# Kernel optimization log

Hardware: AMD Instinct MI355X
Metric: run time of the kernel (lower is better)

## Reference

```python
import jax, jax.numpy as jnp
import numpy as np

N_SYS = 512      # number of crystal systems in the batch
N_ATOM = 32      # atoms per system (uniform for the reference)
N = N_SYS * N_ATOM            # 16384 total atoms
M = N_SYS * N_ATOM * N_ATOM   # 524288 dense intra-system edges
R = 16           # lattice translation points per edge
E = 128          # embed_dim
H = 8            # num_heads


def setup_inputs() -> dict:
    key = jax.random.key(0)
    ks = jax.random.split(key, 6)
    x = jax.random.normal(ks[0], (N, E), jnp.float32)
    in_proj_weight = jax.random.normal(ks[1], (3 * E, E), jnp.float32) / np.float32(np.sqrt(E))
    in_proj_bias = jnp.zeros((3 * E,), jnp.float32)
    out_proj_weight = jax.random.normal(ks[2], (E, E), jnp.float32) / np.float32(np.sqrt(E))
    out_proj_bias = jnp.zeros((E,), jnp.float32)
    # per-node per-head Gaussian exponents; must be negative for convergent lattice sums
    alpha = -(jax.random.uniform(ks[3], (N, H), jnp.float32) * 0.9 + 0.1)
    # squared distances from atom i to lattice images of atom j, up to ~5 Angstrom
    dist2 = jax.random.uniform(ks[4], (M, R), jnp.float32) * 25.0
    # dense intra-system edge list in (query-major) block order, as Crystalformer assumes
    base = (np.arange(N_SYS, dtype=np.int32) * N_ATOM)[:, None, None]
    qi = np.arange(N_ATOM, dtype=np.int32)[None, :, None]
    kj = np.arange(N_ATOM, dtype=np.int32)[None, None, :]
    e0 = np.broadcast_to(base + qi, (N_SYS, N_ATOM, N_ATOM)).reshape(-1)
    e1 = np.broadcast_to(base + kj, (N_SYS, N_ATOM, N_ATOM)).reshape(-1)
    edges = jnp.asarray(np.stack([e0, e1]), jnp.int32)
    batch = jnp.asarray(np.repeat(np.arange(N_SYS, dtype=np.int32), N_ATOM))
    return {
        "x": x,
        "in_proj_weight": in_proj_weight,
        "in_proj_bias": in_proj_bias,
        "out_proj_weight": out_proj_weight,
        "out_proj_bias": out_proj_bias,
        "alpha": alpha,
        "dist2": dist2,
        "edges": edges,
        "batch": batch,
    }


def reference(x, in_proj_weight, in_proj_bias, out_proj_weight, out_proj_bias,
              alpha, dist2, edges, batch):
    n, e = x.shape
    h = alpha.shape[1]
    dh = e // h
    # in-projection (self-attention: q = k = v = x)
    qkv = x @ in_proj_weight.T + in_proj_bias           # [N, 3E]
    q, k, v = jnp.split(qkv, 3, axis=-1)
    q = q.reshape(n, h, dh) / jnp.sqrt(jnp.asarray(dh, x.dtype))
    k = k.reshape(n, h, dh)
    v = v.reshape(n, h, dh)
    e0, e1 = edges[0], edges[1]
    # per-edge dot-product score, gathered q/k  -> [M, H]
    attn = jnp.einsum("mhd,mhd->mh", q[e0], k[e1])
    # real-domain lattice-sum attention bias: logsumexp_r(alpha_i * |r|^2)  -> [M, H]
    aw = jax.nn.logsumexp(alpha[e0][:, :, None] * dist2[:, None, :], axis=-1)
    s = attn + aw
    # segment softmax over each query's neighborhood (norm_func_mode=0 'default')
    smax = jax.ops.segment_max(s, e0, num_segments=n)   # [N, H]
    p = jnp.exp(s - smax[e0])
    denom = jax.ops.segment_sum(p, e0, num_segments=n)  # [N, H]
    p = p / denom[e0]
    # scatter-add aggregation of gathered values  -> [N, H, dh]
    out = jax.ops.segment_sum(p[:, :, None] * v[e1], e0, num_segments=n)
    # out-projection
    out = out.reshape(n, e) @ out_proj_weight.T + out_proj_bias
    return out
```

## Files before the change

kernel.cpp:

```cpp
#include <hip/hip_runtime.h>
#include <hip/hip_bf16.h>

#define LOG2E_F 1.4426950408889634f

typedef __attribute__((ext_vector_type(8))) short short8;
typedef __attribute__((ext_vector_type(4))) float f32x4;

__device__ inline unsigned short f2b(float f) {
    __hip_bfloat16 h = __float2bfloat16(f);
    return *reinterpret_cast<unsigned short*>(&h);
}

__device__ inline short8 load_frag_f32(const float* p) {
    const float4 lo = *(const float4*)p;
    const float4 hi = *(const float4*)(p + 4);
    short8 r;
    r[0] = (short)f2b(lo.x); r[1] = (short)f2b(lo.y);
    r[2] = (short)f2b(lo.z); r[3] = (short)f2b(lo.w);
    r[4] = (short)f2b(hi.x); r[5] = (short)f2b(hi.y);
    r[6] = (short)f2b(hi.z); r[7] = (short)f2b(hi.w);
    return r;
}

__global__ __launch_bounds__(256) void fused_attn_kernel(
    const float* __restrict__ x, const float* __restrict__ Win,
    const float* __restrict__ bin, const float* __restrict__ Wout,
    const float* __restrict__ bout, const float* __restrict__ alpha,
    const float* __restrict__ dist2, float* __restrict__ out)
{
    __shared__ float qkvl[3][32][164];
    __shared__ unsigned short aggb[32][136];

    const int sys  = blockIdx.x;
    const int tid  = threadIdx.x;
    const int lane = tid & 63;
    const int wv   = tid >> 6;
    const int r16  = lane & 15;
    const int kg   = lane >> 4;
    const int base = sys << 5;

    short8 af[2][4];
    #pragma unroll
    for (int rt = 0; rt < 2; ++rt)
        #pragma unroll
        for (int ks = 0; ks < 4; ++ks)
            af[rt][ks] = load_frag_f32(
                x + (size_t)(base + rt * 16 + r16) * 128 + ks * 32 + kg * 8);

    #pragma unroll
    for (int j = 0; j < 6; ++j) {
        const int ct = wv * 6 + j;
        const int c  = ct * 16 + r16;
        short8 bf[4];
        #pragma unroll
        for (int ks = 0; ks < 4; ++ks)
            bf[ks] = load_frag_f32(Win + (size_t)c * 128 + ks * 32 + kg * 8);
        const float bias_v = bin[c];
        const int   bufi   = ct >> 3;
        const int   h      = ct & 7;
        const float scale  = (bufi == 0) ? 0.25f : 1.0f;

        #pragma unroll
        for (int rt = 0; rt < 2; ++rt) {
            f32x4 acc = {0.f, 0.f, 0.f, 0.f};
            #pragma unroll
            for (int ks = 0; ks < 4; ++ks)
                acc = __builtin_amdgcn_mfma_f32_16x16x32_bf16(af[rt][ks], bf[ks], acc, 0, 0, 0);
            #pragma unroll
            for (int r = 0; r < 4; ++r) {
                const int atom = rt * 16 + kg * 4 + r;
                qkvl[bufi][atom][h * 20 + r16] = (acc[r] + bias_v) * scale;
            }
        }
    }

    const int qi = tid >> 3;
    const int h  = tid & 7;
    const float al2 = alpha[(size_t)(base + qi) * 8 + h] * LOG2E_F;

    __syncthreads();

    float qreg[16];
    {
        const float* qrow = &qkvl[0][qi][h * 20];
        #pragma unroll
        for (int d4 = 0; d4 < 4; ++d4) {
            const float4 t = *(const float4*)(qrow + (d4 << 2));
            qreg[d4 * 4 + 0] = t.x; qreg[d4 * 4 + 1] = t.y;
            qreg[d4 * 4 + 2] = t.z; qreg[d4 * 4 + 3] = t.w;
        }
    }

    float m = -1e30f;
    float den = 0.f;
    float acc[16] = {};
    const float* dp = dist2 + (size_t)(sys * 1024 + qi * 32) * 16;

    #pragma unroll 4
    for (int kj = 0; kj < 32; ++kj, dp += 16) {
        const float4 t0 = *(const float4*)(dp + 0);
        const float4 t1 = *(const float4*)(dp + 4);
        const float4 t2 = *(const float4*)(dp + 8);
        const float4 t3 = *(const float4*)(dp + 12);
        const float mn = fminf(
            fminf(fminf(fminf(t0.x, t0.y), fminf(t0.z, t0.w)),
                  fminf(fminf(t1.x, t1.y), fminf(t1.z, t1.w))),
            fminf(fminf(fminf(t2.x, t2.y), fminf(t2.z, t2.w)),
                  fminf(fminf(t3.x, t3.y), fminf(t3.z, t3.w))));
        const float c0 = al2 * mn;
        float e0 = __builtin_amdgcn_exp2f(fmaf(al2, t0.x, -c0));
        e0 += __builtin_amdgcn_exp2f(fmaf(al2, t0.y, -c0));
        e0 += __builtin_amdgcn_exp2f(fmaf(al2, t0.z, -c0));
        e0 += __builtin_amdgcn_exp2f(fmaf(al2, t0.w, -c0));
        float e1 = __builtin_amdgcn_exp2f(fmaf(al2, t1.x, -c0));
        e1 += __builtin_amdgcn_exp2f(fmaf(al2, t1.y, -c0));
        e1 += __builtin_amdgcn_exp2f(fmaf(al2, t1.z, -c0));
        e1 += __builtin_amdgcn_exp2f(fmaf(al2, t1.w, -c0));
        float e2 = __builtin_amdgcn_exp2f(fmaf(al2, t2.x, -c0));
        e2 += __builtin_amdgcn_exp2f(fmaf(al2, t2.y, -c0));
        e2 += __builtin_amdgcn_exp2f(fmaf(al2, t2.z, -c0));
        e2 += __builtin_amdgcn_exp2f(fmaf(al2, t2.w, -c0));
        float e3 = __builtin_amdgcn_exp2f(fmaf(al2, t3.x, -c0));
        e3 += __builtin_amdgcn_exp2f(fmaf(al2, t3.y, -c0));
        e3 += __builtin_amdgcn_exp2f(fmaf(al2, t3.z, -c0));
        e3 += __builtin_amdgcn_exp2f(fmaf(al2, t3.w, -c0));
        const float ssum = (e0 + e1) + (e2 + e3);

        const float* kr = &qkvl[1][kj][h * 20];
        const float4 k0 = *(const float4*)(kr + 0);
        const float4 k1 = *(const float4*)(kr + 4);
        const float4 k2 = *(const float4*)(kr + 8);
        const float4 k3 = *(const float4*)(kr + 12);
        float p0 = qreg[0] * k0.x, p1 = qreg[1] * k0.y;
        float p2 = qreg[2] * k0.z, p3 = qreg[3] * k0.w;
        p0 = fmaf(qreg[4],  k1.x, p0); p1 = fmaf(qreg[5],  k1.y, p1);
        p2 = fmaf(qreg[6],  k1.z, p2); p3 = fmaf(qreg[7],  k1.w, p3);
        p0 = fmaf(qreg[8],  k2.x, p0); p1 = fmaf(qreg[9],  k2.y, p1);
        p2 = fmaf(qreg[10], k2.z, p2); p3 = fmaf(qreg[11], k2.w, p3);
        p0 = fmaf(qreg[12], k3.x, p0); p1 = fmaf(qreg[13], k3.y, p1);
        p2 = fmaf(qreg[14], k3.z, p2); p3 = fmaf(qreg[15], k3.w, p3);
        const float dot = (p0 + p1) + (p2 + p3);

        const float b = fmaf(dot, LOG2E_F, c0);

        if (b - m > 8.0f) {
            const float sc = __builtin_amdgcn_exp2f(m - b);
            den *= sc;
            #pragma unroll
            for (int d = 0; d < 16; ++d) acc[d] *= sc;
            m = b;
        }
        const float p = __builtin_amdgcn_exp2f(b - m) * ssum;
        den += p;

        const float* vr = &qkvl[2][kj][h * 20];
        const float4 v0 = *(const float4*)(vr + 0);
        const float4 v1 = *(const float4*)(vr + 4);
        const float4 v2 = *(const float4*)(vr + 8);
        const float4 v3 = *(const float4*)(vr + 12);
        acc[0]  = fmaf(p, v0.x, acc[0]);  acc[1]  = fmaf(p, v0.y, acc[1]);
        acc[2]  = fmaf(p, v0.z, acc[2]);  acc[3]  = fmaf(p, v0.w, acc[3]);
        acc[4]  = fmaf(p, v1.x, acc[4]);  acc[5]  = fmaf(p, v1.y, acc[5]);
        acc[6]  = fmaf(p, v1.z, acc[6]);  acc[7]  = fmaf(p, v1.w, acc[7]);
        acc[8]  = fmaf(p, v2.x, acc[8]);  acc[9]  = fmaf(p, v2.y, acc[9]);
        acc[10] = fmaf(p, v2.z, acc[10]); acc[11] = fmaf(p, v2.w, acc[11]);
        acc[12] = fmaf(p, v3.x, acc[12]); acc[13] = fmaf(p, v3.y, acc[13]);
        acc[14] = fmaf(p, v3.z, acc[14]); acc[15] = fmaf(p, v3.w, acc[15]);
    }

    {
        const float inv = 1.0f / den;
        unsigned short* op = &aggb[qi][h * 16];
        uint4 o0, o1;
        o0.x = (unsigned)f2b(acc[0]  * inv) | ((unsigned)f2b(acc[1]  * inv) << 16);
        o0.y = (unsigned)f2b(acc[2]  * inv) | ((unsigned)f2b(acc[3]  * inv) << 16);
        o0.z = (unsigned)f2b(acc[4]  * inv) | ((unsigned)f2b(acc[5]  * inv) << 16);
        o0.w = (unsigned)f2b(acc[6]  * inv) | ((unsigned)f2b(acc[7]  * inv) << 16);
        o1.x = (unsigned)f2b(acc[8]  * inv) | ((unsigned)f2b(acc[9]  * inv) << 16);
        o1.y = (unsigned)f2b(acc[10] * inv) | ((unsigned)f2b(acc[11] * inv) << 16);
        o1.z = (unsigned)f2b(acc[12] * inv) | ((unsigned)f2b(acc[13] * inv) << 16);
        o1.w = (unsigned)f2b(acc[14] * inv) | ((unsigned)f2b(acc[15] * inv) << 16);
        *(uint4*)op       = o0;
        *(uint4*)(op + 8) = o1;
    }

    __syncthreads();

    short8 aA[2][4];
    #pragma unroll
    for (int rt = 0; rt < 2; ++rt)
        #pragma unroll
        for (int ks = 0; ks < 4; ++ks)
            aA[rt][ks] = *(const short8*)(&aggb[rt * 16 + r16][ks * 32 + kg * 8]);

    #pragma unroll
    for (int j = 0; j < 2; ++j) {
        const int ct = wv * 2 + j;
        const int c  = ct * 16 + r16;
        short8 bf[4];
        #pragma unroll
        for (int ks = 0; ks < 4; ++ks)
            bf[ks] = load_frag_f32(Wout + (size_t)c * 128 + ks * 32 + kg * 8);
        const float bias_v = bout[c];
        #pragma unroll
        for (int rt = 0; rt < 2; ++rt) {
            f32x4 oacc = {0.f, 0.f, 0.f, 0.f};
            #pragma unroll
            for (int ks = 0; ks < 4; ++ks)
                oacc = __builtin_amdgcn_mfma_f32_16x16x32_bf16(aA[rt][ks], bf[ks], oacc, 0, 0, 0);
            #pragma unroll
            for (int r = 0; r < 4; ++r) {
                const int row = base + rt * 16 + kg * 4 + r;
                out[(size_t)row * 128 + c] = oacc[r] + bias_v;
            }
        }
    }
}

extern "C" void kernel_launch(void* const* d_in, const int* in_sizes, int n_in,
                              void* d_out, int out_size, void* d_ws, size_t ws_size,
                              hipStream_t stream)
{
    const float* x     = (const float*)d_in[0];
    const float* Win   = (const float*)d_in[1];
    const float* bin   = (const float*)d_in[2];
    const float* Wout  = (const float*)d_in[3];
    const float* bout  = (const float*)d_in[4];
    const float* alpha = (const float*)d_in[5];
    const float* dist2 = (const float*)d_in[6];

    fused_attn_kernel<<<dim3(512), 256, 0, stream>>>(
        x, Win, bin, Wout, bout, alpha, dist2, (float*)d_out);
}
```

Before: 43.53 us.

## Double block size and split key loop across two thread halves with softmax merge

Result: faster. 42.14 us (-3.2%).

```diff
diff --git a/kernel.cpp b/kernel.cpp
--- a/kernel.cpp
+++ b/kernel.cpp
@@ -22,7 +22,7 @@
     return r;
 }
 
-__global__ __launch_bounds__(256) void fused_attn_kernel(
+__global__ __launch_bounds__(512, 4) void fused_attn_kernel(
     const float* __restrict__ x, const float* __restrict__ Win,
     const float* __restrict__ bin, const float* __restrict__ Wout,
     const float* __restrict__ bout, const float* __restrict__ alpha,
@@ -48,8 +48,8 @@
                 x + (size_t)(base + rt * 16 + r16) * 128 + ks * 32 + kg * 8);
 
     #pragma unroll
-    for (int j = 0; j < 6; ++j) {
-        const int ct = wv * 6 + j;
+    for (int j = 0; j < 3; ++j) {
+        const int ct = wv * 3 + j;
         const int c  = ct * 16 + r16;
         short8 bf[4];
         #pragma unroll
@@ -57,7 +57,7 @@
             bf[ks] = load_frag_f32(Win + (size_t)c * 128 + ks * 32 + kg * 8);
         const float bias_v = bin[c];
         const int   bufi   = ct >> 3;
-        const int   h      = ct & 7;
+        const int   hh     = ct & 7;
         const float scale  = (bufi == 0) ? 0.25f : 1.0f;
 
         #pragma unroll
@@ -69,13 +69,15 @@
             #pragma unroll
             for (int r = 0; r < 4; ++r) {
                 const int atom = rt * 16 + kg * 4 + r;
-                qkvl[bufi][atom][h * 20 + r16] = (acc[r] + bias_v) * scale;
+                qkvl[bufi][atom][hh * 20 + r16] = (acc[r] + bias_v) * scale;
             }
         }
     }
 
-    const int qi = tid >> 3;
-    const int h  = tid & 7;
+    const int t     = tid & 255;
+    const int khalf = tid >> 8;
+    const int qi    = t >> 3;
+    const int h     = t & 7;
     const float al2 = alpha[(size_t)(base + qi) * 8 + h] * LOG2E_F;
 
     __syncthreads();
@@ -85,19 +87,20 @@
         const float* qrow = &qkvl[0][qi][h * 20];
         #pragma unroll
         for (int d4 = 0; d4 < 4; ++d4) {
-            const float4 t = *(const float4*)(qrow + (d4 << 2));
-            qreg[d4 * 4 + 0] = t.x; qreg[d4 * 4 + 1] = t.y;
-            qreg[d4 * 4 + 2] = t.z; qreg[d4 * 4 + 3] = t.w;
+            const float4 tq = *(const float4*)(qrow + (d4 << 2));
+            qreg[d4 * 4 + 0] = tq.x; qreg[d4 * 4 + 1] = tq.y;
+            qreg[d4 * 4 + 2] = tq.z; qreg[d4 * 4 + 3] = tq.w;
         }
     }
 
     float m = -1e30f;
     float den = 0.f;
     float acc[16] = {};
-    const float* dp = dist2 + (size_t)(sys * 1024 + qi * 32) * 16;
-
-    #pragma unroll 4
-    for (int kj = 0; kj < 32; ++kj, dp += 16) {
+    const float* dp = dist2 + ((size_t)(sys * 1024 + qi * 32) + khalf * 16) * 16;
+
+    #pragma unroll
+    for (int kk = 0; kk < 16; ++kk, dp += 16) {
+        const int kj = khalf * 16 + kk;
         const float4 t0 = *(const float4*)(dp + 0);
         const float4 t1 = *(const float4*)(dp + 4);
         const float4 t2 = *(const float4*)(dp + 8);
@@ -168,18 +171,35 @@
         acc[14] = fmaf(p, v3.z, acc[14]); acc[15] = fmaf(p, v3.w, acc[15]);
     }
 
-    {
-        const float inv = 1.0f / den;
+    __syncthreads();
+    float* exch = &qkvl[0][0][0];
+    if (khalf == 1) {
+        float* e = exch + t * 19;
+        e[0] = m; e[1] = den;
+        #pragma unroll
+        for (int d = 0; d < 16; ++d) e[2 + d] = acc[d];
+    }
+    __syncthreads();
+    if (khalf == 0) {
+        const float* e = exch + t * 19;
+        const float m2   = e[0];
+        const float den2 = e[1];
+        const float M  = fmaxf(m, m2);
+        const float s1 = __builtin_amdgcn_exp2f(m - M);
+        const float s2 = __builtin_amdgcn_exp2f(m2 - M);
+        const float inv = 1.0f / (den * s1 + den2 * s2);
+        const float a1 = s1 * inv, a2 = s2 * inv;
+
         unsigned short* op = &aggb[qi][h * 16];
         uint4 o0, o1;
-        o0.x = (unsigned)f2b(acc[0]  * inv) | ((unsigned)f2b(acc[1]  * inv) << 16);
-        o0.y = (unsigned)f2b(acc[2]  * inv) | ((unsigned)f2b(acc[3]  * inv) << 16);
-        o0.z = (unsigned)f2b(acc[4]  * inv) | ((unsigned)f2b(acc[5]  * inv) << 16);
-        o0.w = (unsigned)f2b(acc[6]  * inv) | ((unsigned)f2b(acc[7]  * inv) << 16);
-        o1.x = (unsigned)f2b(acc[8]  * inv) | ((unsigned)f2b(acc[9]  * inv) << 16);
-        o1.y = (unsigned)f2b(acc[10] * inv) | ((unsigned)f2b(acc[11] * inv) << 16);
-        o1.z = (unsigned)f2b(acc[12] * inv) | ((unsigned)f2b(acc[13] * inv) << 16);
-        o1.w = (unsigned)f2b(acc[14] * inv) | ((unsigned)f2b(acc[15] * inv) << 16);
+        o0.x = (unsigned)f2b(fmaf(acc[0],  a1, e[2]  * a2)) | ((unsigned)f2b(fmaf(acc[1],  a1, e[3]  * a2)) << 16);
+        o0.y = (unsigned)f2b(fmaf(acc[2],  a1, e[4]  * a2)) | ((unsigned)f2b(fmaf(acc[3],  a1, e[5]  * a2)) << 16);
+        o0.z = (unsigned)f2b(fmaf(acc[4],  a1, e[6]  * a2)) | ((unsigned)f2b(fmaf(acc[5],  a1, e[7]  * a2)) << 16);
+        o0.w = (unsigned)f2b(fmaf(acc[6],  a1, e[8]  * a2)) | ((unsigned)f2b(fmaf(acc[7],  a1, e[9]  * a2)) << 16);
+        o1.x = (unsigned)f2b(fmaf(acc[8],  a1, e[10] * a2)) | ((unsigned)f2b(fmaf(acc[9],  a1, e[11] * a2)) << 16);
+        o1.y = (unsigned)f2b(fmaf(acc[10], a1, e[12] * a2)) | ((unsigned)f2b(fmaf(acc[11], a1, e[13] * a2)) << 16);
+        o1.z = (unsigned)f2b(fmaf(acc[12], a1, e[14] * a2)) | ((unsigned)f2b(fmaf(acc[13], a1, e[15] * a2)) << 16);
+        o1.w = (unsigned)f2b(fmaf(acc[14], a1, e[16] * a2)) | ((unsigned)f2b(fmaf(acc[15], a1, e[17] * a2)) << 16);
         *(uint4*)op       = o0;
         *(uint4*)(op + 8) = o1;
     }
@@ -193,10 +213,8 @@
         for (int ks = 0; ks < 4; ++ks)
             aA[rt][ks] = *(const short8*)(&aggb[rt * 16 + r16][ks * 32 + kg * 8]);
 
-    #pragma unroll
-    for (int j = 0; j < 2; ++j) {
-        const int ct = wv * 2 + j;
-        const int c  = ct * 16 + r16;
+    {
+        const int c = wv * 16 + r16;
         short8 bf[4];
         #pragma unroll
         for (int ks = 0; ks < 4; ++ks)
@@ -229,6 +247,6 @@
     const float* alpha = (const float*)d_in[5];
     const float* dist2 = (const float*)d_in[6];
 
-    fused_attn_kernel<<<dim3(512), 256, 0, stream>>>(
+    fused_attn_kernel<<<dim3(512), 512, 0, stream>>>(
         x, Win, bin, Wout, bout, alpha, dist2, (float*)d_out);
 }
```
